# Optimization experiments

Hardware: AMD Instinct MI355X
Metric: run time of the kernel (lower is better)

The kernel has to match this reference:

```python
import jax, jax.numpy as jnp
import numpy as np
import math

T_KER = 1.0
SIGMA = 0.1
COVAR = 5
EPS = 1e-6


def cos_kernel(a, b):
    # a:[B,N,D], b:[B,M,D] -> exp((cos_sim - 1)/T)
    num = jnp.einsum('bnd,bmd->bnm', a, b)
    den = jnp.linalg.norm(a, axis=-1)[..., None] * jnp.linalg.norm(b, axis=-1)[:, None] + EPS
    return jnp.exp((num / den - 1.0) / T_KER)


def get_local_cov(cov, K):
    # cov: [b,h,w,h,w] -> local KxK windows around the diagonal: [b,h,w,K*K]
    b, h, w = cov.shape[0], cov.shape[1], cov.shape[2]
    hw = h * w
    pad = K // 2
    covp = jnp.pad(cov, ((0, 0), (0, 0), (0, 0), (pad, pad), (pad, pad)))
    covp = covp.reshape(b, hw, h + K - 1, w + K - 1)
    dr, dc = np.meshgrid(np.arange(-pad, pad + 1), np.arange(-pad, pad + 1), indexing='ij')
    rb, cb = np.meshgrid(np.arange(pad, pad + h), np.arange(pad, pad + w), indexing='ij')
    rows = (rb[:, :, None, None] + dr[None, None]).reshape(hw, K * K)
    cols = (cb[:, :, None, None] + dc[None, None]).reshape(hw, K * K)
    pts = np.broadcast_to(np.arange(hw)[:, None], (hw, K * K))
    local = covp[:, pts, rows, cols]  # [b,hw,K*K]
    return local.reshape(b, h, w, K * K)


def reference(x, y, pos_w, pos_b):
    b, c, h1, w1 = x.shape
    h2, w2 = y.shape[2], y.shape[3]
    n2 = h2 * w2
    # positional encoding (fourier basis on [-1,1] grid)
    ys = jnp.linspace(-1 + 1 / h2, 1 - 1 / h2, h2)
    xs = jnp.linspace(-1 + 1 / w2, 1 - 1 / w2, w2)
    gy, gx = jnp.meshgrid(ys, xs, indexing='ij')
    coords = jnp.stack([gx, gy], axis=0)  # [2,h2,w2], (x,y) order
    f = jnp.cos(8 * math.pi * (jnp.einsum('dc,chw->dhw', pos_w, coords) + pos_b[:, None, None]))
    d = f.shape[0]
    xf = x.transpose(0, 2, 3, 1).reshape(b, h1 * w1, c)
    yf = y.transpose(0, 2, 3, 1).reshape(b, n2, c)
    ff = jnp.broadcast_to(f.transpose(1, 2, 0).reshape(1, n2, d), (b, n2, d))
    K_yy = cos_kernel(yf, yf)
    K_xy = cos_kernel(xf, yf)
    K_yy_plus = K_yy + SIGMA * jnp.eye(n2, dtype=K_yy.dtype)[None]
    I = jnp.broadcast_to(jnp.eye(n2, dtype=K_yy.dtype), (b, n2, n2))
    K_yy_inv = jnp.linalg.solve(K_yy_plus, I)
    mu = K_xy @ (K_yy_inv @ ff)  # [b, h1*w1, d]
    mu_x = mu.reshape(b, h1, w1, d).transpose(0, 3, 1, 2)
    K_xx = cos_kernel(xf, xf)
    cov = K_xx - K_xy @ (K_yy_inv @ jnp.swapaxes(K_xy, 1, 2))
    cov = cov.reshape(b, h1, w1, h1, w1)
    local = get_local_cov(cov, COVAR).transpose(0, 3, 1, 2)  # [b,K*K,h1,w1]
    return jnp.concatenate([mu_x, local], axis=1)


def setup_inputs() -> dict:
    key = jax.random.key(0)
    k0, k1, k2, k3 = jax.random.split(key, 4)
    return {
        'x': jax.random.normal(k0, (2, 512, 64, 64), dtype=jnp.float32),
        'y': jax.random.normal(k1, (2, 512, 64, 64), dtype=jnp.float32),
        'pos_w': jax.random.normal(k2, (64, 2), dtype=jnp.float32) * 0.5,
        'pos_b': jax.random.normal(k3, (64,), dtype=jnp.float32) * 0.1,
    }
```

## Files before the change

### kernel.cpp

```cpp
#include <hip/hip_runtime.h>
#include <math.h>

#define NPT 4096
#define CCH 512
#define NB 64
#define NKB 64
#define LDB 4160
#define SIGF 0.1f
#define CEPS 1e-6f
#define PI8 25.132741228718345f

#define APSTR ((size_t)2080 * 4096)
#define ILSTR ((size_t)64 * 4096)

typedef __attribute__((ext_vector_type(8))) short bf16x8;
typedef __attribute__((ext_vector_type(4))) float f32x4;
typedef __attribute__((ext_vector_type(4))) unsigned short us4;
typedef unsigned short ushort_t;

__device__ __forceinline__ size_t tbase(int I, int J) {
    return ((size_t)((I * (I + 1) >> 1) + J)) << 12;
}

__device__ inline ushort_t f2bf_rne(float x) {
    unsigned u = __float_as_uint(x);
    unsigned r = u + 0x7FFFu + ((u >> 16) & 1u);
    return (ushort_t)(r >> 16);
}
__device__ inline float bf2f(ushort_t h) { return __uint_as_float(((unsigned)h) << 16); }

__device__ inline void split4(float4 v, us4& h, us4& l) {
    h[0] = f2bf_rne(v.x); l[0] = f2bf_rne(v.x - bf2f(h[0]));
    h[1] = f2bf_rne(v.y); l[1] = f2bf_rne(v.y - bf2f(h[1]));
    h[2] = f2bf_rne(v.z); l[2] = f2bf_rne(v.z - bf2f(h[2]));
    h[3] = f2bf_rne(v.w); l[3] = f2bf_rne(v.w - bf2f(h[3]));
}

__global__ __launch_bounds__(256) void norms_kernel(const float* __restrict__ X,
                                                    float* __restrict__ nrm, int bofs) {
    int slot = blockIdx.y;
    int p = blockIdx.x * 256 + threadIdx.x;
    const float* Xb = X + (size_t)(slot + bofs) * CCH * NPT;
    float s = 0.f;
    #pragma unroll 8
    for (int ch = 0; ch < CCH; ++ch) {
        float v = Xb[(size_t)ch * NPT + p];
        s += v * v;
    }
    nrm[slot * NPT + p] = sqrtf(s);
}

__global__ __launch_bounds__(256) void split_kernel(const float* __restrict__ X,
                                                    ushort_t* __restrict__ Hi,
                                                    ushort_t* __restrict__ Lo,
                                                    int bofs) {
    int ch0 = blockIdx.x * 64, pt0 = blockIdx.y * 64;
    const float* Xb = X + (size_t)bofs * CCH * NPT;
    __shared__ float ls[64][65];
    int tid = threadIdx.x;
    for (int t = tid; t < 4096; t += 256) {
        int chl = t >> 6, ptl = t & 63;
        ls[chl][ptl] = Xb[(size_t)(ch0 + chl) * NPT + pt0 + ptl];
    }
    __syncthreads();
    for (int t = tid; t < 4096; t += 256) {
        int ptl = t >> 6, chl = t & 63;
        float v = ls[chl][ptl];
        ushort_t h = f2bf_rne(v);
        float lo = v - bf2f(h);
        Hi[(size_t)(pt0 + ptl) * CCH + ch0 + chl] = h;
        Lo[(size_t)(pt0 + ptl) * CCH + ch0 + chl] = f2bf_rne(lo);
    }
}

__global__ __launch_bounds__(256) void gramA_packed_kernel(
    const ushort_t* __restrict__ Yhi, const ushort_t* __restrict__ Ylo,
    const float* __restrict__ nY, float* __restrict__ Cp)
{
    int bx = blockIdx.x, by = blockIdx.y;
    if (bx > by) return;
    int bm = by * 128, bn = bx * 128;

    __shared__ __align__(16) ushort_t Ah[128][40];
    __shared__ __align__(16) ushort_t Al[128][40];
    __shared__ __align__(16) ushort_t Bh[128][40];
    __shared__ __align__(16) ushort_t Bl[128][40];

    int tid = threadIdx.x;
    int lane = tid & 63, wid = tid >> 6;
    int wr = wid >> 1, wc = wid & 1;

    f32x4 acc[4][4];
    #pragma unroll
    for (int i = 0; i < 4; ++i)
        #pragma unroll
        for (int j = 0; j < 4; ++j) acc[i][j] = (f32x4){0.f, 0.f, 0.f, 0.f};

    int arr = tid >> 6;
    int srow = lane >> 2, sc4 = lane & 3;
    const ushort_t* src = (arr == 0 || arr == 2) ? Yhi : Ylo;
    int pbase = (arr < 2) ? bm : bn;
    ushort_t* dst = (arr == 0) ? &Ah[0][0] : (arr == 1) ? &Al[0][0] : (arr == 2) ? &Bh[0][0] : &Bl[0][0];

    for (int k0 = 0; k0 < CCH; k0 += 32) {
        #pragma unroll
        for (int it = 0; it < 8; ++it) {
            int row = it * 16 + srow;
            const ushort_t* g = src + (size_t)(pbase + row) * CCH + k0 + sc4 * 8;
            bf16x8 v = *(const bf16x8*)g;
            *(bf16x8*)(dst + row * 40 + sc4 * 8) = v;
        }
        __syncthreads();
        bf16x8 afh[4], afl[4], bfh[4], bfl[4];
        int kcol = (lane >> 4) * 8;
        #pragma unroll
        for (int mi = 0; mi < 4; ++mi) {
            int r = wr * 64 + mi * 16 + (lane & 15);
            afh[mi] = *(const bf16x8*)&Ah[r][kcol];
            afl[mi] = *(const bf16x8*)&Al[r][kcol];
        }
        #pragma unroll
        for (int nj = 0; nj < 4; ++nj) {
            int r = wc * 64 + nj * 16 + (lane & 15);
            bfh[nj] = *(const bf16x8*)&Bh[r][kcol];
            bfl[nj] = *(const bf16x8*)&Bl[r][kcol];
        }
        #pragma unroll
        for (int mi = 0; mi < 4; ++mi)
            #pragma unroll
            for (int nj = 0; nj < 4; ++nj) {
                acc[mi][nj] = __builtin_amdgcn_mfma_f32_16x16x32_bf16(afh[mi], bfh[nj], acc[mi][nj], 0, 0, 0);
                acc[mi][nj] = __builtin_amdgcn_mfma_f32_16x16x32_bf16(afh[mi], bfl[nj], acc[mi][nj], 0, 0, 0);
                acc[mi][nj] = __builtin_amdgcn_mfma_f32_16x16x32_bf16(afl[mi], bfh[nj], acc[mi][nj], 0, 0, 0);
            }
        __syncthreads();
    }

    int I = (bm >> 6) + wr, J = (bn >> 6) + wc;
    if (J > I) return;
    float* Ct = Cp + tbase(I, J);
    #pragma unroll
    for (int nj = 0; nj < 4; ++nj) {
        int cin = nj * 16 + (lane & 15);
        float nbv = nY[bn + wc * 64 + cin];
        #pragma unroll
        for (int mi = 0; mi < 4; ++mi) {
            f32x4 a = acc[mi][nj];
            #pragma unroll
            for (int q = 0; q < 4; ++q) {
                int rin = mi * 16 + (lane >> 4) * 4 + q;
                float den = nY[bm + wr * 64 + rin] * nbv + CEPS;
                float v = expf(a[q] / den - 1.0f);
                if (I == J && rin == cin) v += SIGF;
                Ct[(rin << 6) + cin] = v;
            }
        }
    }
}

__global__ __launch_bounds__(256) void gramX_kernel(
    const ushort_t* __restrict__ Yhi, const ushort_t* __restrict__ Ylo,
    const float* __restrict__ Xf,
    const float* __restrict__ nY, const float* __restrict__ nX,
    float* __restrict__ Cm)
{
    int bm = blockIdx.y * 128, bn = blockIdx.x * 128;

    __shared__ __align__(16) ushort_t Ah[128][40];
    __shared__ __align__(16) ushort_t Al[128][40];
    __shared__ __align__(16) ushort_t Bh[128][40];
    __shared__ __align__(16) ushort_t Bl[128][40];

    int tid = threadIdx.x;
    int lane = tid & 63, wid = tid >> 6;
    int wr = wid >> 1, wc = wid & 1;

    f32x4 acc[4][4];
    #pragma unroll
    for (int i = 0; i < 4; ++i)
        #pragma unroll
        for (int j = 0; j < 4; ++j) acc[i][j] = (f32x4){0.f, 0.f, 0.f, 0.f};

    int srow = lane >> 2, sc4 = lane & 3;

    for (int k0 = 0; k0 < CCH; k0 += 32) {
        if (tid < 128) {
            const ushort_t* src = (tid < 64) ? Yhi : Ylo;
            ushort_t* dst = (tid < 64) ? &Ah[0][0] : &Al[0][0];
            #pragma unroll
            for (int it = 0; it < 8; ++it) {
                int row = it * 16 + srow;
                bf16x8 v = *(const bf16x8*)(src + (size_t)(bm + row) * CCH + k0 + sc4 * 8);
                *(bf16x8*)(dst + row * 40 + sc4 * 8) = v;
            }
        } else {
            int e0 = (tid - 128) * 8;
            #pragma unroll
            for (int i = 0; i < 8; ++i) {
                int e = e0 + i;
                int ch = e >> 5, p4 = e & 31;
                float4 v = *(const float4*)&Xf[(size_t)(k0 + ch) * NPT + bn + (p4 << 2)];
                us4 h, l;
                split4(v, h, l);
                #pragma unroll
                for (int q = 0; q < 4; ++q) {
                    Bh[(p4 << 2) + q][ch] = h[q];
                    Bl[(p4 << 2) + q][ch] = l[q];
                }
            }
        }
        __syncthreads();
        bf16x8 afh[4], afl[4], bfh[4], bfl[4];
        int kcol = (lane >> 4) * 8;
        #pragma unroll
        for (int mi = 0; mi < 4; ++mi) {
            int r = wr * 64 + mi * 16 + (lane & 15);
            afh[mi] = *(const bf16x8*)&Ah[r][kcol];
            afl[mi] = *(const bf16x8*)&Al[r][kcol];
        }
        #pragma unroll
        for (int nj = 0; nj < 4; ++nj) {
            int r = wc * 64 + nj * 16 + (lane & 15);
            bfh[nj] = *(const bf16x8*)&Bh[r][kcol];
            bfl[nj] = *(const bf16x8*)&Bl[r][kcol];
        }
        #pragma unroll
        for (int mi = 0; mi < 4; ++mi)
            #pragma unroll
            for (int nj = 0; nj < 4; ++nj) {
                acc[mi][nj] = __builtin_amdgcn_mfma_f32_16x16x32_bf16(afh[mi], bfh[nj], acc[mi][nj], 0, 0, 0);
                acc[mi][nj] = __builtin_amdgcn_mfma_f32_16x16x32_bf16(afh[mi], bfl[nj], acc[mi][nj], 0, 0, 0);
                acc[mi][nj] = __builtin_amdgcn_mfma_f32_16x16x32_bf16(afl[mi], bfh[nj], acc[mi][nj], 0, 0, 0);
            }
        __syncthreads();
    }

    #pragma unroll
    for (int nj = 0; nj < 4; ++nj) {
        int col = bn + wc * 64 + nj * 16 + (lane & 15);
        float nbv = nX[col];
        #pragma unroll
        for (int mi = 0; mi < 4; ++mi) {
            f32x4 a = acc[mi][nj];
            #pragma unroll
            for (int q = 0; q < 4; ++q) {
                int row = bm + wr * 64 + mi * 16 + (lane >> 4) * 4 + q;
                float den = nY[row] * nbv + CEPS;
                Cm[(size_t)row * LDB + col] = expf(a[q] / den - 1.0f);
            }
        }
    }
}

__global__ __launch_bounds__(256) void features_kernel(const float* __restrict__ pw,
                                                       const float* __restrict__ pb,
                                                       float* __restrict__ Brhs) {
    int g = blockIdx.x * 256 + threadIdx.x;
    int q = g >> 6, dd = g & 63;
    int hh = q >> 6, ww = q & 63;
    float gy = -1.0f + (2 * hh + 1) / 64.0f;
    float gx = -1.0f + (2 * ww + 1) / 64.0f;
    float ph = PI8 * (pw[dd * 2 + 0] * gx + pw[dd * 2 + 1] * gy + pb[dd]);
    Brhs[(size_t)q * LDB + NPT + dd] = cosf(ph);
}

__global__ __launch_bounds__(256) void potf2_packed_kernel(float* __restrict__ AmatP,
                                                           float* __restrict__ invL, int kb) {
    __shared__ float a[NB][NB + 4];
    __shared__ float iv[NB][NB + 4];
    __shared__ float ddiag[NB];
    int slot = blockIdx.z;
    float* Ab = AmatP + (size_t)slot * APSTR + tbase(kb, kb);
    int tid = threadIdx.x;
    int tx = tid & 15, ty = tid >> 4;
    for (int t = tid; t < NB * NB; t += 256) {
        int i = t >> 6, j = t & 63;
        a[i][j] = Ab[(i << 6) + j];
        iv[i][j] = 0.0f;
    }
    __syncthreads();
    for (int j = 0; j < NB; ++j) {
        float ajj = sqrtf(a[j][j]);
        float dinv = 1.0f / ajj;
        if (tid == 0) ddiag[j] = ajj;
        for (int i = j + 1 + tid; i < NB; i += 256) a[i][j] *= dinv;
        for (int c = tid; c <= j; c += 256)
            iv[j][c] = ((c == j ? 1.0f : 0.0f) - iv[j][c]) * dinv;
        __syncthreads();
        for (int i = j + 1 + ty; i < NB; i += 16) {
            float lij = a[i][j];
            for (int jj = j + 1 + tx; jj < NB; jj += 16)
                a[i][jj] -= lij * a[jj][j];
            for (int c = tx; c <= j; c += 16)
                iv[i][c] += lij * iv[j][c];
        }
        __syncthreads();
    }
    float* iL = invL + (size_t)slot * ILSTR + ((size_t)kb << 12);
    for (int t = tid; t < NB * NB; t += 256) {
        int i = t >> 6, j = t & 63;
        if (j < i)       Ab[(i << 6) + j] = a[i][j];
        else if (j == i) Ab[(i << 6) + j] = ddiag[i];
        iL[t] = (j <= i) ? iv[i][j] : 0.0f;
    }
}

__global__ __launch_bounds__(256) void trsm_packed_kernel(float* __restrict__ AmatP,
                                                          const float* __restrict__ invL, int kb) {
    int slot = blockIdx.z;
    int I = kb + 1 + blockIdx.x;
    float* At = AmatP + (size_t)slot * APSTR + tbase(I, kb);
    const float* iL = invL + (size_t)slot * ILSTR + ((size_t)kb << 12);

    __shared__ __align__(16) ushort_t Aoh[64][72], Aol[64][72];
    __shared__ __align__(16) ushort_t Bh[64][72], Bl[64][72];

    int tid = threadIdx.x, lane = tid & 63, w = tid >> 6;
    int frow = lane & 15, fk = (lane >> 4) << 3;
    f32x4 acc[4];
    #pragma unroll
    for (int j = 0; j < 4; ++j) acc[j] = (f32x4){0, 0, 0, 0};

    for (int e = tid; e < 1024; e += 256) {
        int r = e >> 4, k4 = e & 15;
        us4 h, l;
        float4 v = *(const float4*)&At[(r << 6) + (k4 << 2)];
        split4(v, h, l);
        *(us4*)&Aoh[r][k4 << 2] = h; *(us4*)&Aol[r][k4 << 2] = l;
        float4 u = *(const float4*)&iL[(r << 6) + (k4 << 2)];
        split4(u, h, l);
        *(us4*)&Bh[r][k4 << 2] = h; *(us4*)&Bl[r][k4 << 2] = l;
    }
    __syncthreads();
    #pragma unroll
    for (int kk0 = 0; kk0 < 64; kk0 += 32) {
        bf16x8 ah = *(const bf16x8*)&Aoh[(w << 4) + frow][kk0 + fk];
        bf16x8 al = *(const bf16x8*)&Aol[(w << 4) + frow][kk0 + fk];
        #pragma unroll
        for (int nj = 0; nj < 4; ++nj) {
            bf16x8 bh = *(const bf16x8*)&Bh[(nj << 4) + frow][kk0 + fk];
            bf16x8 bl = *(const bf16x8*)&Bl[(nj << 4) + frow][kk0 + fk];
            acc[nj] = __builtin_amdgcn_mfma_f32_16x16x32_bf16(ah, bh, acc[nj], 0, 0, 0);
            acc[nj] = __builtin_amdgcn_mfma_f32_16x16x32_bf16(ah, bl, acc[nj], 0, 0, 0);
            acc[nj] = __builtin_amdgcn_mfma_f32_16x16x32_bf16(al, bh, acc[nj], 0, 0, 0);
        }
    }
    #pragma unroll
    for (int nj = 0; nj < 4; ++nj)
        #pragma unroll
        for (int q = 0; q < 4; ++q) {
            int rin = (w << 4) + ((lane >> 4) << 2) + q;
            At[(rin << 6) + (nj << 4) + frow] = acc[nj][q];
        }
}

__global__ __launch_bounds__(256) void syrk_fact_packed_kernel(float* __restrict__ AmatP,
                                                               float* __restrict__ invL, int kb) {
    int bi = blockIdx.y, bj = blockIdx.x;
    if (bj > bi) return;
    int slot = blockIdx.z;
    int I = kb + 1 + bi, J = kb + 1 + bj;
    float* base = AmatP + (size_t)slot * APSTR;
    const float* Pi_t = base + tbase(I, kb);
    const float* Pj_t = base + tbase(J, kb);
    float* Ct = base + tbase(I, J);

    __shared__ __align__(16) char smem[36864];
    ushort_t (*Pih)[72] = (ushort_t(*)[72])(smem);
    ushort_t (*Pil)[72] = (ushort_t(*)[72])(smem + 9216);
    ushort_t (*Pjh)[72] = (ushort_t(*)[72])(smem + 18432);
    ushort_t (*Pjl)[72] = (ushort_t(*)[72])(smem + 27648);
    float (*fa)[68] = (float(*)[68])(smem);
    float (*fiv)[68] = (float(*)[68])(smem + 17408);
    float* fdd = (float*)(smem + 34816);

    int tid = threadIdx.x, lane = tid & 63, w = tid >> 6;
    int frow = lane & 15, fk = (lane >> 4) << 3;
    f32x4 acc[4];
    #pragma unroll
    for (int j = 0; j < 4; ++j) acc[j] = (f32x4){0, 0, 0, 0};

    for (int e = tid; e < 1024; e += 256) {
        int r = e >> 4, k4 = e & 15;
        us4 h, l;
        float4 v = *(const float4*)&Pi_t[(r << 6) + (k4 << 2)];
        split4(v, h, l);
        *(us4*)&Pih[r][k4 << 2] = h; *(us4*)&Pil[r][k4 << 2] = l;
        float4 u = *(const float4*)&Pj_t[(r << 6) + (k4 << 2)];
        split4(u, h, l);
        *(us4*)&Pjh[r][k4 << 2] = h; *(us4*)&Pjl[r][k4 << 2] = l;
    }
    __syncthreads();
    #pragma unroll
    for (int kk0 = 0; kk0 < 64; kk0 += 32) {
        bf16x8 ah = *(const bf16x8*)&Pih[(w << 4) + frow][kk0 + fk];
        bf16x8 al = *(const bf16x8*)&Pil[(w << 4) + frow][kk0 + fk];
        #pragma unroll
        for (int nj = 0; nj < 4; ++nj) {
            bf16x8 bh = *(const bf16x8*)&Pjh[(nj << 4) + frow][kk0 + fk];
            bf16x8 bl = *(const bf16x8*)&Pjl[(nj << 4) + frow][kk0 + fk];
            acc[nj] = __builtin_amdgcn_mfma_f32_16x16x32_bf16(ah, bh, acc[nj], 0, 0, 0);
            acc[nj] = __builtin_amdgcn_mfma_f32_16x16x32_bf16(ah, bl, acc[nj], 0, 0, 0);
            acc[nj] = __builtin_amdgcn_mfma_f32_16x16x32_bf16(al, bh, acc[nj], 0, 0, 0);
        }
    }

    if (!(bi == 0 && bj == 0)) {
        #pragma unroll
        for (int nj = 0; nj < 4; ++nj) {
            int cin = (nj << 4) + frow;
            #pragma unroll
            for (int q = 0; q < 4; ++q) {
                int rin = (w << 4) + ((lane >> 4) << 2) + q;
                Ct[(rin << 6) + cin] -= acc[nj][q];
            }
        }
        return;
    }

    __syncthreads();
    #pragma unroll
    for (int nj = 0; nj < 4; ++nj) {
        int cin = (nj << 4) + frow;
        #pragma unroll
        for (int q = 0; q < 4; ++q) {
            int rin = (w << 4) + ((lane >> 4) << 2) + q;
            fa[rin][cin] = Ct[(rin << 6) + cin] - acc[nj][q];
            fiv[rin][cin] = 0.0f;
        }
    }
    __syncthreads();
    int tx = tid & 15, ty = tid >> 4;
    for (int j = 0; j < NB; ++j) {
        float ajj = sqrtf(fa[j][j]);
        float dinv = 1.0f / ajj;
        if (tid == 0) fdd[j] = ajj;
        for (int i = j + 1 + tid; i < NB; i += 256) fa[i][j] *= dinv;
        for (int c = tid; c <= j; c += 256)
            fiv[j][c] = ((c == j ? 1.0f : 0.0f) - fiv[j][c]) * dinv;
        __syncthreads();
        for (int i = j + 1 + ty; i < NB; i += 16) {
            float lij = fa[i][j];
            for (int jj = j + 1 + tx; jj < NB; jj += 16)
                fa[i][jj] -= lij * fa[jj][j];
            for (int c = tx; c <= j; c += 16)
                fiv[i][c] += lij * fiv[j][c];
        }
        __syncthreads();
    }
    float* iL = invL + (size_t)slot * ILSTR + ((size_t)(kb + 1) << 12);
    for (int t = tid; t < NB * NB; t += 256) {
        int i = t >> 6, j = t & 63;
        if (j < i)       Ct[(i << 6) + j] = fa[i][j];
        else if (j == i) Ct[(i << 6) + j] = fdd[i];
        iL[t] = (j <= i) ? fiv[i][j] : 0.0f;
    }
}

__global__ __launch_bounds__(256) void trsm_rhs_kernel(float* __restrict__ Brhs,
                                                       const float* __restrict__ invL) {
    int n0 = blockIdx.x * 64;
    __shared__ float invLs[64][68];
    __shared__ float Tds[64][68];
    int tid = threadIdx.x;
    for (int e = tid; e < 1024; e += 256) {
        int r = e >> 4, k4 = e & 15;
        float4 v = *(const float4*)&Brhs[(size_t)r * LDB + n0 + (k4 << 2)];
        int c = k4 << 2;
        Tds[r][c] = v.x; Tds[r][c + 1] = v.y; Tds[r][c + 2] = v.z; Tds[r][c + 3] = v.w;
        float4 u = *(const float4*)&invL[(r << 6) + (k4 << 2)];
        invLs[r][c] = u.x; invLs[r][c + 1] = u.y; invLs[r][c + 2] = u.z; invLs[r][c + 3] = u.w;
    }
    __syncthreads();
    int col = tid & 63, rg = tid >> 6;
    #pragma unroll
    for (int i = 0; i < 16; ++i) {
        int r = (i << 2) + rg;
        float s = 0.f;
        #pragma unroll 16
        for (int k = 0; k < 64; ++k) s += invLs[r][k] * Tds[k][col];
        Brhs[(size_t)r * LDB + n0 + col] = s;
    }
}

__global__ __launch_bounds__(256) void solve_step_kernel(const float* __restrict__ AmatP,
                                                         float* __restrict__ Brhs,
                                                         const float* __restrict__ invL, int kb) {
    int n0 = blockIdx.x * 64;
    int I = kb + 1 + blockIdx.y;
    int rb = kb * NB;
    int ri = I * NB;
    const float* Lt = AmatP + tbase(I, kb);

    __shared__ __align__(16) char smem[36864];
    ushort_t (*Lh)[72] = (ushort_t(*)[72])(smem);
    ushort_t (*Ll)[72] = (ushort_t(*)[72])(smem + 9216);
    ushort_t (*Uh)[72] = (ushort_t(*)[72])(smem + 18432);
    ushort_t (*Ul)[72] = (ushort_t(*)[72])(smem + 27648);
    float (*invLs)[68] = (float(*)[68])(smem);
    float (*Tds)[68]   = (float(*)[68])(smem + 18432);

    int tid = threadIdx.x, lane = tid & 63, w = tid >> 6;
    int frow = lane & 15, fk = (lane >> 4) << 3;

    for (int e = tid; e < 1024; e += 256) {
        int r = e >> 4, k4 = e & 15;
        us4 h, l;
        float4 v = *(const float4*)&Lt[(r << 6) + (k4 << 2)];
        split4(v, h, l);
        *(us4*)&Lh[r][k4 << 2] = h; *(us4*)&Ll[r][k4 << 2] = l;
        float4 u = *(const float4*)&Brhs[(size_t)(rb + r) * LDB + n0 + (k4 << 2)];
        split4(u, h, l);
        #pragma unroll
        for (int q = 0; q < 4; ++q) {
            Uh[(k4 << 2) + q][r] = h[q];
            Ul[(k4 << 2) + q][r] = l[q];
        }
    }
    __syncthreads();

    f32x4 acc[4];
    #pragma unroll
    for (int j = 0; j < 4; ++j) acc[j] = (f32x4){0, 0, 0, 0};
    #pragma unroll
    for (int kk0 = 0; kk0 < 64; kk0 += 32) {
        bf16x8 ah = *(const bf16x8*)&Lh[(w << 4) + frow][kk0 + fk];
        bf16x8 al = *(const bf16x8*)&Ll[(w << 4) + frow][kk0 + fk];
        #pragma unroll
        for (int nj = 0; nj < 4; ++nj) {
            bf16x8 bh = *(const bf16x8*)&Uh[(nj << 4) + frow][kk0 + fk];
            bf16x8 bl = *(const bf16x8*)&Ul[(nj << 4) + frow][kk0 + fk];
            acc[nj] = __builtin_amdgcn_mfma_f32_16x16x32_bf16(ah, bh, acc[nj], 0, 0, 0);
            acc[nj] = __builtin_amdgcn_mfma_f32_16x16x32_bf16(ah, bl, acc[nj], 0, 0, 0);
            acc[nj] = __builtin_amdgcn_mfma_f32_16x16x32_bf16(al, bh, acc[nj], 0, 0, 0);
        }
    }

    if (blockIdx.y > 0) {
        #pragma unroll
        for (int nj = 0; nj < 4; ++nj) {
            int cin = (nj << 4) + frow;
            #pragma unroll
            for (int q = 0; q < 4; ++q) {
                int rin = (w << 4) + ((lane >> 4) << 2) + q;
                Brhs[(size_t)(ri + rin) * LDB + n0 + cin] -= acc[nj][q];
            }
        }
        return;
    }

    __syncthreads();
    #pragma unroll
    for (int nj = 0; nj < 4; ++nj) {
        int cin = (nj << 4) + frow;
        #pragma unroll
        for (int q = 0; q < 4; ++q) {
            int rin = (w << 4) + ((lane >> 4) << 2) + q;
            Tds[rin][cin] = Brhs[(size_t)(ri + rin) * LDB + n0 + cin] - acc[nj][q];
        }
    }
    const float* iL = invL + ((size_t)(kb + 1) << 12);
    for (int e = tid; e < 1024; e += 256) {
        int r = e >> 4, k4 = e & 15;
        float4 u = *(const float4*)&iL[(r << 6) + (k4 << 2)];
        int c = k4 << 2;
        invLs[r][c] = u.x; invLs[r][c + 1] = u.y; invLs[r][c + 2] = u.z; invLs[r][c + 3] = u.w;
    }
    __syncthreads();
    int col = tid & 63, rg = tid >> 6;
    #pragma unroll
    for (int i = 0; i < 16; ++i) {
        int r = (i << 2) + rg;
        float s = 0.f;
        #pragma unroll 16
        for (int k = 0; k < 64; ++k) s += invLs[r][k] * Tds[k][col];
        Brhs[(size_t)(ri + r) * LDB + n0 + col] = s;
    }
}

__global__ __launch_bounds__(256) void mu_kernel(const float* __restrict__ Brhs,
                                                 float* __restrict__ out, int bofs) {
    const float* Bb = Brhs;
    int p0 = blockIdx.x * 64;
    __shared__ float Us[16][65];
    __shared__ float Vs[16][65];
    float acc[4][4] = {};
    int tid = threadIdx.x, tx = tid & 15, ty = tid >> 4;
    for (int q0 = 0; q0 < NPT; q0 += 16) {
        for (int t = tid; t < 1024; t += 256) {
            int kk = t >> 6, c = t & 63;
            Us[kk][c] = Bb[(size_t)(q0 + kk) * LDB + p0 + c];
            Vs[kk][c] = Bb[(size_t)(q0 + kk) * LDB + NPT + c];
        }
        __syncthreads();
        #pragma unroll
        for (int kk = 0; kk < 16; ++kk) {
            float uv[4], vv[4];
            #pragma unroll
            for (int i = 0; i < 4; ++i) { uv[i] = Us[kk][ty * 4 + i]; vv[i] = Vs[kk][tx * 4 + i]; }
            #pragma unroll
            for (int i = 0; i < 4; ++i)
                #pragma unroll
                for (int j = 0; j < 4; ++j) acc[i][j] += uv[i] * vv[j];
        }
        __syncthreads();
    }
    #pragma unroll
    for (int i = 0; i < 4; ++i)
        #pragma unroll
        for (int j = 0; j < 4; ++j)
            out[((size_t)bofs * 89 + tx * 4 + j) * NPT + p0 + ty * 4 + i] = acc[i][j];
}

__global__ __launch_bounds__(256) void kxx_local_kernel(const float* __restrict__ X,
                                                        const float* __restrict__ nxb,
                                                        float* __restrict__ tmp, int bofs) {
    int r = blockIdx.y;
    int c0 = blockIdx.x * 16;
    const float* Xb = X + (size_t)bofs * CCH * NPT;
    __shared__ float Xs[32][104];
    int tid = threadIdx.x;
    int t0 = tid, t1 = tid + 256;
    int pl0 = t0 / 25, jj0 = t0 % 25;
    int pl1 = t1 / 25, jj1 = t1 % 25;
    int pidx0 = 40 + pl0 + 2;
    int jidx0 = (jj0 / 5) * 20 + pl0 + (jj0 % 5);
    int pidx1 = 40 + pl1 + 2;
    int jidx1 = (jj1 / 5) * 20 + pl1 + (jj1 % 5);
    float acc0 = 0.f, acc1 = 0.f;
    for (int ch0 = 0; ch0 < CCH; ch0 += 32) {
        for (int t = tid; t < 32 * 100; t += 256) {
            int ch = t / 100, i = t % 100;
            int s = i / 20, cc = i % 20;
            int gr = r + s - 2, gc = c0 - 2 + cc;
            float v = 0.f;
            if (gr >= 0 && gr < 64 && gc >= 0 && gc < 64)
                v = Xb[(size_t)(ch0 + ch) * NPT + gr * 64 + gc];
            Xs[ch][i] = v;
        }
        __syncthreads();
        #pragma unroll 8
        for (int kk = 0; kk < 32; ++kk) {
            acc0 += Xs[kk][pidx0] * Xs[kk][jidx0];
            if (t1 < 400) acc1 += Xs[kk][pidx1] * Xs[kk][jidx1];
        }
        __syncthreads();
    }
    {
        int p = r * 64 + c0 + pl0;
        int qr = r + jj0 / 5 - 2, qc = c0 + pl0 + jj0 % 5 - 2;
        float v = 0.f;
        if (qr >= 0 && qr < 64 && qc >= 0 && qc < 64) {
            int q = qr * 64 + qc;
            v = expf(acc0 / (nxb[p] * nxb[q] + CEPS) - 1.0f);
        }
        tmp[(size_t)jj0 * NPT + p] = v;
    }
    if (t1 < 400) {
        int p = r * 64 + c0 + pl1;
        int qr = r + jj1 / 5 - 2, qc = c0 + pl1 + jj1 % 5 - 2;
        float v = 0.f;
        if (qr >= 0 && qr < 64 && qc >= 0 && qc < 64) {
            int q = qr * 64 + qc;
            v = expf(acc1 / (nxb[p] * nxb[q] + CEPS) - 1.0f);
        }
        tmp[(size_t)jj1 * NPT + p] = v;
    }
}

__global__ __launch_bounds__(256) void cov_local_kernel(const float* __restrict__ Brhs,
                                                        const float* __restrict__ tmp,
                                                        float* __restrict__ out, int bofs) {
    int r = blockIdx.y;
    int c0 = blockIdx.x * 16;
    const float* Ub = Brhs;
    __shared__ float Us[64][104];
    int tid = threadIdx.x;
    int t0 = tid, t1 = tid + 256;
    int pl0 = t0 / 25, jj0 = t0 % 25;
    int pl1 = t1 / 25, jj1 = t1 % 25;
    int pidx0 = 40 + pl0 + 2;
    int jidx0 = (jj0 / 5) * 20 + pl0 + (jj0 % 5);
    int pidx1 = 40 + pl1 + 2;
    int jidx1 = (jj1 / 5) * 20 + pl1 + (jj1 % 5);
    float acc0 = 0.f, acc1 = 0.f;
    for (int q0 = 0; q0 < NPT; q0 += 64) {
        for (int t = tid; t < 64 * 100; t += 256) {
            int qq = t / 100, i = t % 100;
            int s = i / 20, cc = i % 20;
            int gr = r + s - 2, gc = c0 - 2 + cc;
            float v = 0.f;
            if (gr >= 0 && gr < 64 && gc >= 0 && gc < 64)
                v = Ub[(size_t)(q0 + qq) * LDB + gr * 64 + gc];
            Us[qq][i] = v;
        }
        __syncthreads();
        #pragma unroll 8
        for (int kk = 0; kk < 64; ++kk) {
            acc0 += Us[kk][pidx0] * Us[kk][jidx0];
            if (t1 < 400) acc1 += Us[kk][pidx1] * Us[kk][jidx1];
        }
        __syncthreads();
    }
    {
        int p = r * 64 + c0 + pl0;
        int qr = r + jj0 / 5 - 2, qc = c0 + pl0 + jj0 % 5 - 2;
        float v = 0.f;
        if (qr >= 0 && qr < 64 && qc >= 0 && qc < 64)
            v = tmp[(size_t)jj0 * NPT + p] - acc0;
        out[((size_t)bofs * 89 + 64 + jj0) * NPT + p] = v;
    }
    if (t1 < 400) {
        int p = r * 64 + c0 + pl1;
        int qr = r + jj1 / 5 - 2, qc = c0 + pl1 + jj1 % 5 - 2;
        float v = 0.f;
        if (qr >= 0 && qr < 64 && qc >= 0 && qc < 64)
            v = tmp[(size_t)jj1 * NPT + p] - acc1;
        out[((size_t)bofs * 89 + 64 + jj1) * NPT + p] = v;
    }
}

extern "C" void kernel_launch(void* const* d_in, const int* in_sizes, int n_in,
                              void* d_out, int out_size, void* d_ws, size_t ws_size,
                              hipStream_t stream) {
    (void)in_sizes; (void)n_in; (void)out_size;
    const float* x  = (const float*)d_in[0];
    const float* y  = (const float*)d_in[1];
    const float* pw = (const float*)d_in[2];
    const float* pb = (const float*)d_in[3];
    float* out = (float*)d_out;
    float* ws  = (float*)d_ws;

    const size_t NEED = 2 * APSTR + (size_t)NPT * LDB + 2 * ILSTR + 4 * NPT + 2 * ((size_t)NPT * CCH / 2);
    if (ws_size < NEED * sizeof(float)) return;

    float* AmatP = ws;
    float* Brhs  = AmatP + 2 * APSTR;
    float* invL  = Brhs + (size_t)NPT * LDB;
    float* nx    = invL + 2 * ILSTR;
    float* ny    = nx + 2 * NPT;
    float* ysBuf = ny + 2 * NPT;
    ushort_t* ysH = (ushort_t*)ysBuf;
    ushort_t* ysL = ysH + (size_t)NPT * CCH;
    float* tmp = invL;

    norms_kernel<<<dim3(16, 2), 256, 0, stream>>>(x, nx, 0);
    norms_kernel<<<dim3(16, 2), 256, 0, stream>>>(y, ny, 0);

    for (int b = 0; b < 2; ++b) {
        split_kernel<<<dim3(8, 64, 1), 256, 0, stream>>>(y, ysH, ysL, b);
        gramA_packed_kernel<<<dim3(32, 32, 1), 256, 0, stream>>>(
            ysH, ysL, ny + (size_t)b * NPT, AmatP + (size_t)b * APSTR);
    }

    potf2_packed_kernel<<<dim3(1, 1, 2), 256, 0, stream>>>(AmatP, invL, 0);
    for (int kb = 0; kb < NKB - 1; ++kb) {
        int nt = NKB - 1 - kb;
        trsm_packed_kernel<<<dim3(nt, 1, 2), 256, 0, stream>>>(AmatP, invL, kb);
        syrk_fact_packed_kernel<<<dim3(nt, nt, 2), 256, 0, stream>>>(AmatP, invL, kb);
    }

    for (int b = 0; b < 2; ++b) {
        split_kernel<<<dim3(8, 64, 1), 256, 0, stream>>>(y, ysH, ysL, b);
        features_kernel<<<dim3(1024, 1), 256, 0, stream>>>(pw, pb, Brhs);
        gramX_kernel<<<dim3(32, 32, 1), 256, 0, stream>>>(
            ysH, ysL, x + (size_t)b * CCH * NPT, ny + (size_t)b * NPT, nx + (size_t)b * NPT, Brhs);

        trsm_rhs_kernel<<<dim3(65, 1, 1), 256, 0, stream>>>(Brhs, invL + (size_t)b * ILSTR);
        for (int kb = 0; kb < NKB - 1; ++kb) {
            solve_step_kernel<<<dim3(65, NKB - 1 - kb, 1), 256, 0, stream>>>(
                AmatP + (size_t)b * APSTR, Brhs, invL + (size_t)b * ILSTR, kb);
        }

        mu_kernel<<<dim3(64, 1, 1), 256, 0, stream>>>(Brhs, out, b);
        kxx_local_kernel<<<dim3(4, 64, 1), 256, 0, stream>>>(x, nx + (size_t)b * NPT, tmp, b);
        cov_local_kernel<<<dim3(4, 64, 1), 256, 0, stream>>>(Brhs, tmp, out, b);
    }
}
```

Baseline: 11.39 ms.

## Fuse TRSM into SYRK step and batch both triangular solves per launch

Removes the separate TRSM launch in the blocked Cholesky. Each SYRK block now recomputes its panel tiles as raw A times the diagonal inverse on the fly, instead of reading panels already written back in place. This halves the launch count and the grid-wide sync points per step, at the cost of redundant panel multiplies across blocks and larger shared memory. Separately, when the workspace allows, the forward solve runs both batches in one launch using a second RHS buffer, which doubles the blocks per solve step. The solve kernel also applies the diagonal inverse to the unmodified L panel internally.

```diff
diff --git a/kernel.cpp b/kernel.cpp
--- a/kernel.cpp
+++ b/kernel.cpp
@@ -106,8 +106,7 @@
         #pragma unroll
         for (int it = 0; it < 8; ++it) {
             int row = it * 16 + srow;
-            const ushort_t* g = src + (size_t)(pbase + row) * CCH + k0 + sc4 * 8;
-            bf16x8 v = *(const bf16x8*)g;
+            bf16x8 v = *(const bf16x8*)(src + (size_t)(pbase + row) * CCH + k0 + sc4 * 8);
             *(bf16x8*)(dst + row * 40 + sc4 * 8) = v;
         }
         __syncthreads();
@@ -305,103 +304,108 @@
     }
 }
 
-__global__ __launch_bounds__(256) void trsm_packed_kernel(float* __restrict__ AmatP,
-                                                          const float* __restrict__ invL, int kb) {
-    int slot = blockIdx.z;
-    int I = kb + 1 + blockIdx.x;
-    float* At = AmatP + (size_t)slot * APSTR + tbase(I, kb);
-    const float* iL = invL + (size_t)slot * ILSTR + ((size_t)kb << 12);
-
-    __shared__ __align__(16) ushort_t Aoh[64][72], Aol[64][72];
-    __shared__ __align__(16) ushort_t Bh[64][72], Bl[64][72];
-
-    int tid = threadIdx.x, lane = tid & 63, w = tid >> 6;
-    int frow = lane & 15, fk = (lane >> 4) << 3;
-    f32x4 acc[4];
-    #pragma unroll
-    for (int j = 0; j < 4; ++j) acc[j] = (f32x4){0, 0, 0, 0};
-
-    for (int e = tid; e < 1024; e += 256) {
-        int r = e >> 4, k4 = e & 15;
-        us4 h, l;
-        float4 v = *(const float4*)&At[(r << 6) + (k4 << 2)];
-        split4(v, h, l);
-        *(us4*)&Aoh[r][k4 << 2] = h; *(us4*)&Aol[r][k4 << 2] = l;
-        float4 u = *(const float4*)&iL[(r << 6) + (k4 << 2)];
-        split4(u, h, l);
-        *(us4*)&Bh[r][k4 << 2] = h; *(us4*)&Bl[r][k4 << 2] = l;
-    }
-    __syncthreads();
-    #pragma unroll
-    for (int kk0 = 0; kk0 < 64; kk0 += 32) {
-        bf16x8 ah = *(const bf16x8*)&Aoh[(w << 4) + frow][kk0 + fk];
-        bf16x8 al = *(const bf16x8*)&Aol[(w << 4) + frow][kk0 + fk];
-        #pragma unroll
-        for (int nj = 0; nj < 4; ++nj) {
-            bf16x8 bh = *(const bf16x8*)&Bh[(nj << 4) + frow][kk0 + fk];
-            bf16x8 bl = *(const bf16x8*)&Bl[(nj << 4) + frow][kk0 + fk];
-            acc[nj] = __builtin_amdgcn_mfma_f32_16x16x32_bf16(ah, bh, acc[nj], 0, 0, 0);
-            acc[nj] = __builtin_amdgcn_mfma_f32_16x16x32_bf16(ah, bl, acc[nj], 0, 0, 0);
-            acc[nj] = __builtin_amdgcn_mfma_f32_16x16x32_bf16(al, bh, acc[nj], 0, 0, 0);
-        }
-    }
-    #pragma unroll
-    for (int nj = 0; nj < 4; ++nj)
-        #pragma unroll
-        for (int q = 0; q < 4; ++q) {
-            int rin = (w << 4) + ((lane >> 4) << 2) + q;
-            At[(rin << 6) + (nj << 4) + frow] = acc[nj][q];
-        }
-}
-
-__global__ __launch_bounds__(256) void syrk_fact_packed_kernel(float* __restrict__ AmatP,
-                                                               float* __restrict__ invL, int kb) {
+__global__ __launch_bounds__(256) void chol_step_kernel(float* __restrict__ AmatP,
+                                                        float* __restrict__ invL, int kb) {
     int bi = blockIdx.y, bj = blockIdx.x;
     if (bj > bi) return;
     int slot = blockIdx.z;
     int I = kb + 1 + bi, J = kb + 1 + bj;
     float* base = AmatP + (size_t)slot * APSTR;
-    const float* Pi_t = base + tbase(I, kb);
-    const float* Pj_t = base + tbase(J, kb);
+    const float* Ai = base + tbase(I, kb);
+    const float* Aj = base + tbase(J, kb);
     float* Ct = base + tbase(I, J);
-
-    __shared__ __align__(16) char smem[36864];
-    ushort_t (*Pih)[72] = (ushort_t(*)[72])(smem);
-    ushort_t (*Pil)[72] = (ushort_t(*)[72])(smem + 9216);
-    ushort_t (*Pjh)[72] = (ushort_t(*)[72])(smem + 18432);
-    ushort_t (*Pjl)[72] = (ushort_t(*)[72])(smem + 27648);
-    float (*fa)[68] = (float(*)[68])(smem);
-    float (*fiv)[68] = (float(*)[68])(smem + 17408);
-    float* fdd = (float*)(smem + 34816);
+    const float* iLk = invL + (size_t)slot * ILSTR + ((size_t)kb << 12);
+
+    __shared__ __align__(16) char smem[55296];
+    ushort_t (*iLh)[72] = (ushort_t(*)[72])(smem);
+    ushort_t (*iLl)[72] = (ushort_t(*)[72])(smem + 9216);
+    ushort_t (*Pih)[72] = (ushort_t(*)[72])(smem + 18432);
+    ushort_t (*Pil)[72] = (ushort_t(*)[72])(smem + 27648);
+    ushort_t (*Pjh)[72] = (ushort_t(*)[72])(smem + 36864);
+    ushort_t (*Pjl)[72] = (ushort_t(*)[72])(smem + 46080);
+    float (*fa)[68]  = (float(*)[68])(smem + 36864);
+    float (*fiv)[68] = (float(*)[68])(smem);
+    float* fdd = (float*)(smem + 18432);
 
     int tid = threadIdx.x, lane = tid & 63, w = tid >> 6;
     int frow = lane & 15, fk = (lane >> 4) << 3;
-    f32x4 acc[4];
-    #pragma unroll
-    for (int j = 0; j < 4; ++j) acc[j] = (f32x4){0, 0, 0, 0};
+    int diag = (bi == bj);
 
     for (int e = tid; e < 1024; e += 256) {
         int r = e >> 4, k4 = e & 15;
         us4 h, l;
-        float4 v = *(const float4*)&Pi_t[(r << 6) + (k4 << 2)];
+        float4 v = *(const float4*)&iLk[(r << 6) + (k4 << 2)];
+        split4(v, h, l);
+        *(us4*)&iLh[r][k4 << 2] = h; *(us4*)&iLl[r][k4 << 2] = l;
+        v = *(const float4*)&Ai[(r << 6) + (k4 << 2)];
         split4(v, h, l);
         *(us4*)&Pih[r][k4 << 2] = h; *(us4*)&Pil[r][k4 << 2] = l;
-        float4 u = *(const float4*)&Pj_t[(r << 6) + (k4 << 2)];
-        split4(u, h, l);
-        *(us4*)&Pjh[r][k4 << 2] = h; *(us4*)&Pjl[r][k4 << 2] = l;
-    }
-    __syncthreads();
+        if (!diag) {
+            v = *(const float4*)&Aj[(r << 6) + (k4 << 2)];
+            split4(v, h, l);
+            *(us4*)&Pjh[r][k4 << 2] = h; *(us4*)&Pjl[r][k4 << 2] = l;
+        }
+    }
+    __syncthreads();
+
+    f32x4 aPi[4], aPj[4];
+    #pragma unroll
+    for (int j = 0; j < 4; ++j) { aPi[j] = (f32x4){0, 0, 0, 0}; aPj[j] = (f32x4){0, 0, 0, 0}; }
     #pragma unroll
     for (int kk0 = 0; kk0 < 64; kk0 += 32) {
         bf16x8 ah = *(const bf16x8*)&Pih[(w << 4) + frow][kk0 + fk];
         bf16x8 al = *(const bf16x8*)&Pil[(w << 4) + frow][kk0 + fk];
+        bf16x8 ajh = *(const bf16x8*)&Pjh[(w << 4) + frow][kk0 + fk];
+        bf16x8 ajl = *(const bf16x8*)&Pjl[(w << 4) + frow][kk0 + fk];
         #pragma unroll
         for (int nj = 0; nj < 4; ++nj) {
-            bf16x8 bh = *(const bf16x8*)&Pjh[(nj << 4) + frow][kk0 + fk];
-            bf16x8 bl = *(const bf16x8*)&Pjl[(nj << 4) + frow][kk0 + fk];
-            acc[nj] = __builtin_amdgcn_mfma_f32_16x16x32_bf16(ah, bh, acc[nj], 0, 0, 0);
-            acc[nj] = __builtin_amdgcn_mfma_f32_16x16x32_bf16(ah, bl, acc[nj], 0, 0, 0);
-            acc[nj] = __builtin_amdgcn_mfma_f32_16x16x32_bf16(al, bh, acc[nj], 0, 0, 0);
+            bf16x8 bh = *(const bf16x8*)&iLh[(nj << 4) + frow][kk0 + fk];
+            bf16x8 bl = *(const bf16x8*)&iLl[(nj << 4) + frow][kk0 + fk];
+            aPi[nj] = __builtin_amdgcn_mfma_f32_16x16x32_bf16(ah, bh, aPi[nj], 0, 0, 0);
+            aPi[nj] = __builtin_amdgcn_mfma_f32_16x16x32_bf16(ah, bl, aPi[nj], 0, 0, 0);
+            aPi[nj] = __builtin_amdgcn_mfma_f32_16x16x32_bf16(al, bh, aPi[nj], 0, 0, 0);
+            if (!diag) {
+                aPj[nj] = __builtin_amdgcn_mfma_f32_16x16x32_bf16(ajh, bh, aPj[nj], 0, 0, 0);
+                aPj[nj] = __builtin_amdgcn_mfma_f32_16x16x32_bf16(ajh, bl, aPj[nj], 0, 0, 0);
+                aPj[nj] = __builtin_amdgcn_mfma_f32_16x16x32_bf16(ajl, bh, aPj[nj], 0, 0, 0);
+            }
+        }
+    }
+    __syncthreads();
+    #pragma unroll
+    for (int nj = 0; nj < 4; ++nj) {
+        int cin = (nj << 4) + frow;
+        #pragma unroll
+        for (int q = 0; q < 4; ++q) {
+            int rin = (w << 4) + ((lane >> 4) << 2) + q;
+            float v = aPi[nj][q];
+            ushort_t h = f2bf_rne(v);
+            Pih[rin][cin] = h; Pil[rin][cin] = f2bf_rne(v - bf2f(h));
+            if (!diag) {
+                float u = aPj[nj][q];
+                ushort_t h2 = f2bf_rne(u);
+                Pjh[rin][cin] = h2; Pjl[rin][cin] = f2bf_rne(u - bf2f(h2));
+            }
+        }
+    }
+    __syncthreads();
+
+    const ushort_t (*Bsh)[72] = diag ? Pih : Pjh;
+    const ushort_t (*Bsl)[72] = diag ? Pil : Pjl;
+    f32x4 aC[4];
+    #pragma unroll
+    for (int j = 0; j < 4; ++j) aC[j] = (f32x4){0, 0, 0, 0};
+    #pragma unroll
+    for (int kk0 = 0; kk0 < 64; kk0 += 32) {
+        bf16x8 ah = *(const bf16x8*)&Pih[(w << 4) + frow][kk0 + fk];
+        bf16x8 al = *(const bf16x8*)&Pil[(w << 4) + frow][kk0 + fk];
+        #pragma unroll
+        for (int nj = 0; nj < 4; ++nj) {
+            bf16x8 bh = *(const bf16x8*)&Bsh[(nj << 4) + frow][kk0 + fk];
+            bf16x8 bl = *(const bf16x8*)&Bsl[(nj << 4) + frow][kk0 + fk];
+            aC[nj] = __builtin_amdgcn_mfma_f32_16x16x32_bf16(ah, bh, aC[nj], 0, 0, 0);
+            aC[nj] = __builtin_amdgcn_mfma_f32_16x16x32_bf16(ah, bl, aC[nj], 0, 0, 0);
+            aC[nj] = __builtin_amdgcn_mfma_f32_16x16x32_bf16(al, bh, aC[nj], 0, 0, 0);
         }
     }
 
@@ -412,7 +416,7 @@
             #pragma unroll
             for (int q = 0; q < 4; ++q) {
                 int rin = (w << 4) + ((lane >> 4) << 2) + q;
-                Ct[(rin << 6) + cin] -= acc[nj][q];
+                Ct[(rin << 6) + cin] -= aC[nj][q];
             }
         }
         return;
@@ -425,7 +429,7 @@
         #pragma unroll
         for (int q = 0; q < 4; ++q) {
             int rin = (w << 4) + ((lane >> 4) << 2) + q;
-            fa[rin][cin] = Ct[(rin << 6) + cin] - acc[nj][q];
+            fa[rin][cin] = Ct[(rin << 6) + cin] - aC[nj][q];
             fiv[rin][cin] = 0.0f;
         }
     }
@@ -448,27 +452,30 @@
         }
         __syncthreads();
     }
-    float* iL = invL + (size_t)slot * ILSTR + ((size_t)(kb + 1) << 12);
+    float* iLo = invL + (size_t)slot * ILSTR + ((size_t)(kb + 1) << 12);
     for (int t = tid; t < NB * NB; t += 256) {
         int i = t >> 6, j = t & 63;
-        if (j < i)       Ct[(i << 6) + j] = fa[i][j];
-        else if (j == i) Ct[(i << 6) + j] = fdd[i];
-        iL[t] = (j <= i) ? fiv[i][j] : 0.0f;
-    }
+        iLo[t] = (j <= i) ? fiv[i][j] : 0.0f;
+    }
+    (void)fdd;
 }
 
 __global__ __launch_bounds__(256) void trsm_rhs_kernel(float* __restrict__ Brhs,
-                                                       const float* __restrict__ invL) {
+                                                       const float* __restrict__ invL,
+                                                       size_t brStride) {
+    int slot = blockIdx.z;
+    float* Bb = Brhs + (size_t)slot * brStride;
+    const float* iL = invL + (size_t)slot * ILSTR;
     int n0 = blockIdx.x * 64;
     __shared__ float invLs[64][68];
     __shared__ float Tds[64][68];
     int tid = threadIdx.x;
     for (int e = tid; e < 1024; e += 256) {
         int r = e >> 4, k4 = e & 15;
-        float4 v = *(const float4*)&Brhs[(size_t)r * LDB + n0 + (k4 << 2)];
+        float4 v = *(const float4*)&Bb[(size_t)r * LDB + n0 + (k4 << 2)];
         int c = k4 << 2;
         Tds[r][c] = v.x; Tds[r][c + 1] = v.y; Tds[r][c + 2] = v.z; Tds[r][c + 3] = v.w;
-        float4 u = *(const float4*)&invL[(r << 6) + (k4 << 2)];
+        float4 u = *(const float4*)&iL[(r << 6) + (k4 << 2)];
         invLs[r][c] = u.x; invLs[r][c + 1] = u.y; invLs[r][c + 2] = u.z; invLs[r][c + 3] = u.w;
     }
     __syncthreads();
@@ -479,42 +486,82 @@
         float s = 0.f;
         #pragma unroll 16
         for (int k = 0; k < 64; ++k) s += invLs[r][k] * Tds[k][col];
-        Brhs[(size_t)r * LDB + n0 + col] = s;
+        Bb[(size_t)r * LDB + n0 + col] = s;
     }
 }
 
 __global__ __launch_bounds__(256) void solve_step_kernel(const float* __restrict__ AmatP,
                                                          float* __restrict__ Brhs,
-                                                         const float* __restrict__ invL, int kb) {
+                                                         const float* __restrict__ invL,
+                                                         size_t brStride, int kb) {
+    int slot = blockIdx.z;
     int n0 = blockIdx.x * 64;
     int I = kb + 1 + blockIdx.y;
     int rb = kb * NB;
     int ri = I * NB;
-    const float* Lt = AmatP + tbase(I, kb);
-
-    __shared__ __align__(16) char smem[36864];
-    ushort_t (*Lh)[72] = (ushort_t(*)[72])(smem);
-    ushort_t (*Ll)[72] = (ushort_t(*)[72])(smem + 9216);
-    ushort_t (*Uh)[72] = (ushort_t(*)[72])(smem + 18432);
-    ushort_t (*Ul)[72] = (ushort_t(*)[72])(smem + 27648);
+    const float* Araw = AmatP + (size_t)slot * APSTR + tbase(I, kb);
+    const float* iLbase = invL + (size_t)slot * ILSTR;
+    float* Bb = Brhs + (size_t)slot * brStride;
+
+    __shared__ __align__(16) char smem[55296];
+    ushort_t (*Lh)[72]  = (ushort_t(*)[72])(smem);
+    ushort_t (*Ll)[72]  = (ushort_t(*)[72])(smem + 9216);
+    ushort_t (*iLh)[72] = (ushort_t(*)[72])(smem + 18432);
+    ushort_t (*iLl)[72] = (ushort_t(*)[72])(smem + 27648);
+    ushort_t (*Uh)[72]  = (ushort_t(*)[72])(smem + 36864);
+    ushort_t (*Ul)[72]  = (ushort_t(*)[72])(smem + 46080);
     float (*invLs)[68] = (float(*)[68])(smem);
     float (*Tds)[68]   = (float(*)[68])(smem + 18432);
 
     int tid = threadIdx.x, lane = tid & 63, w = tid >> 6;
     int frow = lane & 15, fk = (lane >> 4) << 3;
 
+    const float* iLk = iLbase + ((size_t)kb << 12);
     for (int e = tid; e < 1024; e += 256) {
         int r = e >> 4, k4 = e & 15;
         us4 h, l;
-        float4 v = *(const float4*)&Lt[(r << 6) + (k4 << 2)];
+        float4 v = *(const float4*)&Araw[(r << 6) + (k4 << 2)];
         split4(v, h, l);
         *(us4*)&Lh[r][k4 << 2] = h; *(us4*)&Ll[r][k4 << 2] = l;
-        float4 u = *(const float4*)&Brhs[(size_t)(rb + r) * LDB + n0 + (k4 << 2)];
+        v = *(const float4*)&iLk[(r << 6) + (k4 << 2)];
+        split4(v, h, l);
+        *(us4*)&iLh[r][k4 << 2] = h; *(us4*)&iLl[r][k4 << 2] = l;
+        float4 u = *(const float4*)&Bb[(size_t)(rb + r) * LDB + n0 + (k4 << 2)];
         split4(u, h, l);
         #pragma unroll
         for (int q = 0; q < 4; ++q) {
             Uh[(k4 << 2) + q][r] = h[q];
             Ul[(k4 << 2) + q][r] = l[q];
+        }
+    }
+    __syncthreads();
+
+    f32x4 aP[4];
+    #pragma unroll
+    for (int j = 0; j < 4; ++j) aP[j] = (f32x4){0, 0, 0, 0};
+    #pragma unroll
+    for (int kk0 = 0; kk0 < 64; kk0 += 32) {
+        bf16x8 ah = *(const bf16x8*)&Lh[(w << 4) + frow][kk0 + fk];
+        bf16x8 al = *(const bf16x8*)&Ll[(w << 4) + frow][kk0 + fk];
+        #pragma unroll
+        for (int nj = 0; nj < 4; ++nj) {
+            bf16x8 bh = *(const bf16x8*)&iLh[(nj << 4) + frow][kk0 + fk];
+            bf16x8 bl = *(const bf16x8*)&iLl[(nj << 4) + frow][kk0 + fk];
+            aP[nj] = __builtin_amdgcn_mfma_f32_16x16x32_bf16(ah, bh, aP[nj], 0, 0, 0);
+            aP[nj] = __builtin_amdgcn_mfma_f32_16x16x32_bf16(ah, bl, aP[nj], 0, 0, 0);
+            aP[nj] = __builtin_amdgcn_mfma_f32_16x16x32_bf16(al, bh, aP[nj], 0, 0, 0);
+        }
+    }
+    __syncthreads();
+    #pragma unroll
+    for (int nj = 0; nj < 4; ++nj) {
+        int cin = (nj << 4) + frow;
+        #pragma unroll
+        for (int q = 0; q < 4; ++q) {
+            int rin = (w << 4) + ((lane >> 4) << 2) + q;
+            float v = aP[nj][q];
+            ushort_t h = f2bf_rne(v);
+            Lh[rin][cin] = h; Ll[rin][cin] = f2bf_rne(v - bf2f(h));
         }
     }
     __syncthreads();
@@ -543,7 +590,7 @@
             #pragma unroll
             for (int q = 0; q < 4; ++q) {
                 int rin = (w << 4) + ((lane >> 4) << 2) + q;
-                Brhs[(size_t)(ri + rin) * LDB + n0 + cin] -= acc[nj][q];
+                Bb[(size_t)(ri + rin) * LDB + n0 + cin] -= acc[nj][q];
             }
         }
         return;
@@ -556,13 +603,13 @@
         #pragma unroll
         for (int q = 0; q < 4; ++q) {
             int rin = (w << 4) + ((lane >> 4) << 2) + q;
-            Tds[rin][cin] = Brhs[(size_t)(ri + rin) * LDB + n0 + cin] - acc[nj][q];
-        }
-    }
-    const float* iL = invL + ((size_t)(kb + 1) << 12);
+            Tds[rin][cin] = Bb[(size_t)(ri + rin) * LDB + n0 + cin] - acc[nj][q];
+        }
+    }
+    const float* iL2 = iLbase + ((size_t)(kb + 1) << 12);
     for (int e = tid; e < 1024; e += 256) {
         int r = e >> 4, k4 = e & 15;
-        float4 u = *(const float4*)&iL[(r << 6) + (k4 << 2)];
+        float4 u = *(const float4*)&iL2[(r << 6) + (k4 << 2)];
         int c = k4 << 2;
         invLs[r][c] = u.x; invLs[r][c + 1] = u.y; invLs[r][c + 2] = u.z; invLs[r][c + 3] = u.w;
     }
@@ -574,7 +621,7 @@
         float s = 0.f;
         #pragma unroll 16
         for (int k = 0; k < 64; ++k) s += invLs[r][k] * Tds[k][col];
-        Brhs[(size_t)(ri + r) * LDB + n0 + col] = s;
+        Bb[(size_t)(ri + r) * LDB + n0 + col] = s;
     }
 }
 
@@ -731,12 +778,15 @@
     float* out = (float*)d_out;
     float* ws  = (float*)d_ws;
 
-    const size_t NEED = 2 * APSTR + (size_t)NPT * LDB + 2 * ILSTR + 4 * NPT + 2 * ((size_t)NPT * CCH / 2);
-    if (ws_size < NEED * sizeof(float)) return;
+    const size_t SZ_B = (size_t)NPT * LDB;
+    const size_t NEED1 = 2 * APSTR + SZ_B + 2 * ILSTR + 4 * NPT + (size_t)NPT * CCH;
+    const size_t NEED2 = NEED1 + SZ_B;
+    if (ws_size < NEED1 * sizeof(float)) return;
+    int twoB = (ws_size >= NEED2 * sizeof(float)) ? 1 : 0;
 
     float* AmatP = ws;
     float* Brhs  = AmatP + 2 * APSTR;
-    float* invL  = Brhs + (size_t)NPT * LDB;
+    float* invL  = Brhs + (size_t)(twoB ? 2 : 1) * SZ_B;
     float* nx    = invL + 2 * ILSTR;
     float* ny    = nx + 2 * NPT;
     float* ysBuf = ny + 2 * NPT;
@@ -756,24 +806,42 @@
     potf2_packed_kernel<<<dim3(1, 1, 2), 256, 0, stream>>>(AmatP, invL, 0);
     for (int kb = 0; kb < NKB - 1; ++kb) {
         int nt = NKB - 1 - kb;
-        trsm_packed_kernel<<<dim3(nt, 1, 2), 256, 0, stream>>>(AmatP, invL, kb);
-        syrk_fact_packed_kernel<<<dim3(nt, nt, 2), 256, 0, stream>>>(AmatP, invL, kb);
-    }
-
-    for (int b = 0; b < 2; ++b) {
-        split_kernel<<<dim3(8, 64, 1), 256, 0, stream>>>(y, ysH, ysL, b);
-        features_kernel<<<dim3(1024, 1), 256, 0, stream>>>(pw, pb, Brhs);
-        gramX_kernel<<<dim3(32, 32, 1), 256, 0, stream>>>(
-            ysH, ysL, x + (size_t)b * CCH * NPT, ny + (size_t)b * NPT, nx + (size_t)b * NPT, Brhs);
-
-        trsm_rhs_kernel<<<dim3(65, 1, 1), 256, 0, stream>>>(Brhs, invL + (size_t)b * ILSTR);
+        chol_step_kernel<<<dim3(nt, nt, 2), 256, 0, stream>>>(AmatP, invL, kb);
+    }
+
+    if (twoB) {
+        for (int b = 0; b < 2; ++b) {
+            split_kernel<<<dim3(8, 64, 1), 256, 0, stream>>>(y, ysH, ysL, b);
+            features_kernel<<<dim3(1024, 1), 256, 0, stream>>>(pw, pb, Brhs + (size_t)b * SZ_B);
+            gramX_kernel<<<dim3(32, 32, 1), 256, 0, stream>>>(
+                ysH, ysL, x + (size_t)b * CCH * NPT, ny + (size_t)b * NPT, nx + (size_t)b * NPT,
+                Brhs + (size_t)b * SZ_B);
+        }
+        trsm_rhs_kernel<<<dim3(65, 1, 2), 256, 0, stream>>>(Brhs, invL, SZ_B);
         for (int kb = 0; kb < NKB - 1; ++kb) {
-            solve_step_kernel<<<dim3(65, NKB - 1 - kb, 1), 256, 0, stream>>>(
-                AmatP + (size_t)b * APSTR, Brhs, invL + (size_t)b * ILSTR, kb);
-        }
-
-        mu_kernel<<<dim3(64, 1, 1), 256, 0, stream>>>(Brhs, out, b);
-        kxx_local_kernel<<<dim3(4, 64, 1), 256, 0, stream>>>(x, nx + (size_t)b * NPT, tmp, b);
-        cov_local_kernel<<<dim3(4, 64, 1), 256, 0, stream>>>(Brhs, tmp, out, b);
-    }
-}
+            solve_step_kernel<<<dim3(65, NKB - 1 - kb, 2), 256, 0, stream>>>(
+                AmatP, Brhs, invL, SZ_B, kb);
+        }
+        for (int b = 0; b < 2; ++b) {
+            float* Bb = Brhs + (size_t)b * SZ_B;
+            mu_kernel<<<dim3(64, 1, 1), 256, 0, stream>>>(Bb, out, b);
+            kxx_local_kernel<<<dim3(4, 64, 1), 256, 0, stream>>>(x, nx + (size_t)b * NPT, tmp, b);
+            cov_local_kernel<<<dim3(4, 64, 1), 256, 0, stream>>>(Bb, tmp, out, b);
+        }
+    } else {
+        for (int b = 0; b < 2; ++b) {
+            split_kernel<<<dim3(8, 64, 1), 256, 0, stream>>>(y, ysH, ysL, b);
+            features_kernel<<<dim3(1024, 1), 256, 0, stream>>>(pw, pb, Brhs);
+            gramX_kernel<<<dim3(32, 32, 1), 256, 0, stream>>>(
+                ysH, ysL, x + (size_t)b * CCH * NPT, ny + (size_t)b * NPT, nx + (size_t)b * NPT, Brhs);
+            trsm_rhs_kernel<<<dim3(65, 1, 1), 256, 0, stream>>>(Brhs, invL + (size_t)b * ILSTR, 0);
+            for (int kb = 0; kb < NKB - 1; ++kb) {
+                solve_step_kernel<<<dim3(65, NKB - 1 - kb, 1), 256, 0, stream>>>(
+                    AmatP + (size_t)b * APSTR, Brhs, invL + (size_t)b * ILSTR, 0, kb);
+            }
+            mu_kernel<<<dim3(64, 1, 1), 256, 0, stream>>>(Brhs, out, b);
+            kxx_local_kernel<<<dim3(4, 64, 1), 256, 0, stream>>>(x, nx + (size_t)b * NPT, tmp, b);
+            cov_local_kernel<<<dim3(4, 64, 1), 256, 0, stream>>>(Brhs, tmp, out, b);
+        }
+    }
+}
```

After: 12.20 ms. +7.1%, slower.
